# Optimization experiments

Hardware: AMD Instinct MI355X
Metric: run time of the kernel (lower is better)

The kernel has to match this reference:

```python
import jax, jax.numpy as jnp
import numpy as np

B, S, U = 4, 4096, 1024

def setup_inputs() -> dict:
    key = jax.random.key(0)
    ks = jax.random.split(key, 8)
    scale = 1.0 / np.sqrt(U)
    return {
        "query": jax.random.normal(ks[0], (B, S, U), dtype=jnp.float32),
        "key": jax.random.normal(ks[1], (B, S, U), dtype=jnp.float32),
        "value": jax.random.normal(ks[2], (B, S, U), dtype=jnp.float32),
        "mask": jnp.ones((B, S, 1), dtype=jnp.float32),
        "Wk": jax.random.normal(ks[3], (U, U), dtype=jnp.float32) * scale,
        "Wv": jax.random.normal(ks[4], (U, U), dtype=jnp.float32) * scale,
        "Wq": jax.random.normal(ks[5], (U, U), dtype=jnp.float32) * scale,
        "Wo": jax.random.normal(ks[6], (U, U), dtype=jnp.float32) * scale,
    }

def reference(query, key, value, mask, Wk, Wv, Wq, Wo):
    # Dense projections (no bias), per the keras layer
    pk = jnp.einsum('bsu,uv->bsv', key, Wk)
    pv = jnp.einsum('bsu,uv->bsv', value, Wv)
    pq = jnp.einsum('bsu,uv->bsv', query, Wq)
    # mask applied BEFORE swish on k, and to v
    pk = pk * mask
    pv = pv * mask
    pk = jax.nn.swish(pk)
    # kv = K^T V : [B, U, U]; out = Q @ kv : [B, S, U]
    kv = jnp.einsum('bsu,bsv->buv', pk, pv)
    out = jnp.einsum('bsu,buv->bsv', pq, kv)
    return jnp.einsum('bsu,uv->bsv', out, Wo)
```

## Files before the change

kernel.cpp:

```cpp
#include <hip/hip_runtime.h>
#include <cstdint>


typedef unsigned short u16;
typedef unsigned int   u32;
typedef float  f32x4  __attribute__((ext_vector_type(4)));
typedef __bf16 bf16x8 __attribute__((ext_vector_type(8)));
typedef u32    u32x4  __attribute__((ext_vector_type(4)));
typedef u16    u16x4  __attribute__((ext_vector_type(4)));

__device__ __forceinline__ u16 f2bf(float f) {
  u32 u = __builtin_bit_cast(u32, f);
  u = (u + 0x7FFFu + ((u >> 16) & 1u)) >> 16;
  return (u16)u;
}
__device__ __forceinline__ u32 pack2(float a, float b) {
  return (u32)f2bf(a) | ((u32)f2bf(b) << 16);
}

template<int EPI, int AF32>
__global__ __launch_bounds__(256)
void gemm_nt(const void* __restrict__ Aptr, const u16* __restrict__ Bptr,
             void* __restrict__ Cptr, const float* __restrict__ maskp,
             int M, int N, int K, int ldA, int ldB,
             long batchA, long batchB, long batchC)
{
  __shared__ u16 As[128 * 64];
  __shared__ u16 Bs[128 * 64];

  const int t    = threadIdx.x;
  const int z    = blockIdx.z;
  const int m0   = blockIdx.y * 128;
  const int n0   = blockIdx.x * 128;
  const int lane = t & 63;
  const int w    = t >> 6, wr = w >> 1, wc = w & 1;
  const int g    = lane >> 4, r16 = lane & 15;
  const int srow = t >> 3, sk8 = t & 7;
  const int swz_w = (sk8 ^ (srow & 7)) << 4;
  const int swz_r = (r16 & 7) << 4;

  const float* Af = (const float*)Aptr + (AF32 ? batchA * (long)z : 0);
  const u16*   Ab = (const u16*)Aptr   + (AF32 ? 0 : batchA * (long)z);
  const u16*   Bb = Bptr + batchB * (long)z;

  f32x4 acc[4][4];
  {
    f32x4 z4;
    for (int q = 0; q < 4; ++q) z4[q] = 0.f;
    #pragma unroll
    for (int i = 0; i < 4; ++i)
      #pragma unroll
      for (int j = 0; j < 4; ++j) acc[i][j] = z4;
  }

  f32x4 raf[4][2];
  u32x4 ra[4];
  u32x4 rb[4];

  auto LOAD = [&](int kt) {
    const long kcol = (long)kt * 64 + sk8 * 8;
    #pragma unroll
    for (int i = 0; i < 4; ++i) {
      const long arow = m0 + i * 32 + srow;
      if constexpr (AF32) {
        const float* p = Af + arow * (long)ldA + kcol;
        raf[i][0] = *(const f32x4*)p;
        raf[i][1] = *(const f32x4*)(p + 4);
      } else {
        const u16* p = Ab + arow * (long)ldA + kcol;
        ra[i] = *(const u32x4*)p;
      }
      const long brow = n0 + i * 32 + srow;
      rb[i] = *(const u32x4*)(Bb + brow * (long)ldB + kcol);
    }
  };

  auto STORE_LDS = [&]() {
    #pragma unroll
    for (int i = 0; i < 4; ++i) {
      const int off = (i * 32 + srow) * 128 + swz_w;
      if constexpr (AF32) {
        u32x4 v;
        v[0] = pack2(raf[i][0][0], raf[i][0][1]);
        v[1] = pack2(raf[i][0][2], raf[i][0][3]);
        v[2] = pack2(raf[i][1][0], raf[i][1][1]);
        v[3] = pack2(raf[i][1][2], raf[i][1][3]);
        *(u32x4*)((char*)As + off) = v;
      } else {
        *(u32x4*)((char*)As + off) = ra[i];
      }
      *(u32x4*)((char*)Bs + off) = rb[i];
    }
  };

  auto COMPUTE = [&]() {
    #pragma unroll
    for (int kk = 0; kk < 2; ++kk) {
      bf16x8 af[4], bfv[4];
      #pragma unroll
      for (int m = 0; m < 4; ++m) {
        const int row  = wr * 64 + m * 16 + r16;
        const int koff = (((kk * 4 + g) << 4) ^ swz_r);
        af[m] = *(const bf16x8*)((const char*)As + row * 128 + koff);
      }
      #pragma unroll
      for (int n = 0; n < 4; ++n) {
        const int row  = wc * 64 + n * 16 + r16;
        const int koff = (((kk * 4 + g) << 4) ^ swz_r);
        bfv[n] = *(const bf16x8*)((const char*)Bs + row * 128 + koff);
      }
      #pragma unroll
      for (int m = 0; m < 4; ++m)
        #pragma unroll
        for (int n = 0; n < 4; ++n)
          acc[m][n] = __builtin_amdgcn_mfma_f32_16x16x32_bf16(af[m], bfv[n], acc[m][n], 0, 0, 0);
    }
  };

  const int nk = K / 64;
  LOAD(0);
  for (int kt = 0;; ++kt) {
    __syncthreads();
    STORE_LDS();
    __syncthreads();
    if (kt + 1 < nk) LOAD(kt + 1);
    COMPUTE();
    if (kt + 1 >= nk) break;
  }

  if constexpr (EPI <= 1) {
    u16* C = (u16*)Cptr + batchC * (long)z;
    const float* mz = maskp + (long)z * M;
    #pragma unroll
    for (int m = 0; m < 4; ++m) {
      const int sbase = m0 + wr * 64 + m * 16 + 4 * g;
      float mk[4];
      #pragma unroll
      for (int j = 0; j < 4; ++j) mk[j] = mz[sbase + j];
      #pragma unroll
      for (int n = 0; n < 4; ++n) {
        const int col = n0 + wc * 64 + n * 16 + r16;
        u16x4 v;
        #pragma unroll
        for (int j = 0; j < 4; ++j) {
          float x = acc[m][n][j] * mk[j];
          if constexpr (EPI == 0) x = x / (1.f + __expf(-x));
          v[j] = f2bf(x);
        }
        *(u16x4*)(C + (long)col * M + sbase) = v;
      }
    }
  } else if constexpr (EPI == 2) {
    u16* C = (u16*)Cptr + batchC * (long)z;
    #pragma unroll
    for (int m = 0; m < 4; ++m) {
      const int rbase = m0 + wr * 64 + m * 16 + 4 * g;
      #pragma unroll
      for (int n = 0; n < 4; ++n) {
        const int col = n0 + wc * 64 + n * 16 + r16;
        #pragma unroll
        for (int j = 0; j < 4; ++j)
          C[(long)(rbase + j) * N + col] = f2bf(acc[m][n][j]);
      }
    }
  } else {
    float* C = (float*)Cptr + batchC * (long)z;
    #pragma unroll
    for (int m = 0; m < 4; ++m) {
      const int rbase = m0 + wr * 64 + m * 16 + 4 * g;
      #pragma unroll
      for (int n = 0; n < 4; ++n) {
        const int col = n0 + wc * 64 + n * 16 + r16;
        #pragma unroll
        for (int j = 0; j < 4; ++j)
          C[(long)(rbase + j) * N + col] = acc[m][n][j];
      }
    }
  }
}

__global__ void tconv_kernel(const float* __restrict__ src, u16* __restrict__ dst)
{
  __shared__ float tile[32][33];
  const int tx = threadIdx.x, ty = threadIdx.y;
  const int c0 = blockIdx.x * 32, r0 = blockIdx.y * 32;
  #pragma unroll
  for (int j = 0; j < 4; ++j)
    tile[ty * 4 + j][tx] = src[(long)(r0 + ty * 4 + j) * 1024 + c0 + tx];
  __syncthreads();
  #pragma unroll
  for (int j = 0; j < 4; ++j)
    dst[(long)(c0 + ty * 4 + j) * 1024 + r0 + tx] = f2bf(tile[tx][ty * 4 + j]);
}

__global__ void conv_kernel(const float* __restrict__ src, u16* __restrict__ dst, int n8)
{
  const int i = blockIdx.x * blockDim.x + threadIdx.x;
  if (i < n8) {
    const f32x4 a = *(const f32x4*)(src + (long)i * 8);
    const f32x4 b = *(const f32x4*)(src + (long)i * 8 + 4);
    u32x4 v;
    v[0] = pack2(a[0], a[1]);
    v[1] = pack2(a[2], a[3]);
    v[2] = pack2(b[0], b[1]);
    v[3] = pack2(b[2], b[3]);
    *(u32x4*)(dst + (long)i * 8) = v;
  }
}

extern "C" void kernel_launch(void* const* d_in, const int* in_sizes, int n_in,
                              void* d_out, int out_size, void* d_ws, size_t ws_size,
                              hipStream_t stream)
{
  const float* q    = (const float*)d_in[0];
  const float* k    = (const float*)d_in[1];
  const float* v    = (const float*)d_in[2];
  const float* mask = (const float*)d_in[3];
  const float* Wk   = (const float*)d_in[4];
  const float* Wv   = (const float*)d_in[5];
  const float* Wq   = (const float*)d_in[6];
  const float* Wo   = (const float*)d_in[7];

  const int B = 4, S = 4096, U = 1024;
  const long SU = (long)S * U;
  const long UU = (long)U * U;

  char* ws = (char*)d_ws;
  u16* pkT = (u16*)(ws);
  u16* pvT = (u16*)(ws + (32l << 20));
  u16* WkT = (u16*)(ws + (64l << 20));
  u16* WvT = (u16*)(ws + (66l << 20));
  u16* Wqb = (u16*)(ws + (68l << 20));
  u16* WoT = (u16*)(ws + (70l << 20));
  u16* kvT = (u16*)(ws + (72l << 20));
  u16* Wtm = (u16*)(ws + (80l << 20));
  u16* WfT = (u16*)(ws + (88l << 20));

  const dim3 blk(256);

  tconv_kernel<<<dim3(32, 32), dim3(32, 8), 0, stream>>>(Wk, WkT);
  tconv_kernel<<<dim3(32, 32), dim3(32, 8), 0, stream>>>(Wv, WvT);
  tconv_kernel<<<dim3(32, 32), dim3(32, 8), 0, stream>>>(Wo, WoT);
  conv_kernel<<<512, 256, 0, stream>>>(Wq, Wqb, (int)(UU / 8));

  gemm_nt<0, 1><<<dim3(8, 32, 4), blk, 0, stream>>>(k, WkT, pkT, mask,
      S, U, U, U, U, SU, 0, SU);
  gemm_nt<1, 1><<<dim3(8, 32, 4), blk, 0, stream>>>(v, WvT, pvT, mask,
      S, U, U, U, U, SU, 0, SU);
  gemm_nt<2, 0><<<dim3(8, 8, 4), blk, 0, stream>>>(pvT, pkT, kvT, nullptr,
      U, U, S, S, S, SU, SU, UU);
  gemm_nt<2, 0><<<dim3(8, 8, 4), blk, 0, stream>>>(Wqb, kvT, Wtm, nullptr,
      U, U, U, U, U, 0, UU, UU);
  gemm_nt<2, 0><<<dim3(8, 8, 4), blk, 0, stream>>>(WoT, Wtm, WfT, nullptr,
      U, U, U, U, U, 0, UU, UU);
  gemm_nt<3, 1><<<dim3(8, 32, 4), blk, 0, stream>>>(q, WfT, d_out, nullptr,
      S, U, U, U, U, SU, UU, SU);
}
```

Measured before the change: 504.5 us.

## Load GEMM tiles directly into LDS and pre-convert activations to bf16

The GEMM kernel now fills LDS with direct global-to-LDS 16-byte loads (global_load_lds) instead of staging through registers. It drops the XOR swizzle and the register prefetch of the next k-tile, so each iteration loads, waits, then computes. To allow this, the fp32 query/key/value inputs are first converted to bf16 by separate conversion passes, using the output buffer and freed workspace as scratch. The aim is to cut register staging and VGPR pressure. The costs are extra full-tensor conversion traffic, no load/compute overlap, and likely LDS bank conflicts on the unswizzled reads.

```diff
diff --git a/kernel.cpp b/kernel.cpp
--- a/kernel.cpp
+++ b/kernel.cpp
@@ -18,9 +18,16 @@
   return (u32)f2bf(a) | ((u32)f2bf(b) << 16);
 }
 
-template<int EPI, int AF32>
+__device__ __forceinline__ void gld_lds16(const u16* g, u16* l) {
+  __builtin_amdgcn_global_load_lds(
+      (const __attribute__((address_space(1))) void*)g,
+      (__attribute__((address_space(3))) void*)l,
+      16, 0, 0);
+}
+
+template<int EPI>
 __global__ __launch_bounds__(256)
-void gemm_nt(const void* __restrict__ Aptr, const u16* __restrict__ Bptr,
+void gemm_nt(const u16* __restrict__ Aptr, const u16* __restrict__ Bptr,
              void* __restrict__ Cptr, const float* __restrict__ maskp,
              int M, int N, int K, int ldA, int ldB,
              long batchA, long batchB, long batchC)
@@ -35,13 +42,15 @@
   const int lane = t & 63;
   const int w    = t >> 6, wr = w >> 1, wc = w & 1;
   const int g    = lane >> 4, r16 = lane & 15;
-  const int srow = t >> 3, sk8 = t & 7;
-  const int swz_w = (sk8 ^ (srow & 7)) << 4;
-  const int swz_r = (r16 & 7) << 4;
-
-  const float* Af = (const float*)Aptr + (AF32 ? batchA * (long)z : 0);
-  const u16*   Ab = (const u16*)Aptr   + (AF32 ? 0 : batchA * (long)z);
-  const u16*   Bb = Bptr + batchB * (long)z;
+  const int lrow = lane >> 3, lch = lane & 7;
+
+  const u16* Ab = Aptr + batchA * (long)z;
+  const u16* Bb = Bptr + batchB * (long)z;
+
+  const u16* pA = Ab + (long)(m0 + w * 32 + lrow) * ldA + lch * 8;
+  const u16* pB = Bb + (long)(n0 + w * 32 + lrow) * ldB + lch * 8;
+  u16* lA = As + w * 2048;
+  u16* lB = Bs + w * 2048;
 
   f32x4 acc[4][4];
   {
@@ -53,60 +62,30 @@
       for (int j = 0; j < 4; ++j) acc[i][j] = z4;
   }
 
-  f32x4 raf[4][2];
-  u32x4 ra[4];
-  u32x4 rb[4];
-
-  auto LOAD = [&](int kt) {
-    const long kcol = (long)kt * 64 + sk8 * 8;
-    #pragma unroll
-    for (int i = 0; i < 4; ++i) {
-      const long arow = m0 + i * 32 + srow;
-      if constexpr (AF32) {
-        const float* p = Af + arow * (long)ldA + kcol;
-        raf[i][0] = *(const f32x4*)p;
-        raf[i][1] = *(const f32x4*)(p + 4);
-      } else {
-        const u16* p = Ab + arow * (long)ldA + kcol;
-        ra[i] = *(const u32x4*)p;
-      }
-      const long brow = n0 + i * 32 + srow;
-      rb[i] = *(const u32x4*)(Bb + brow * (long)ldB + kcol);
-    }
-  };
-
-  auto STORE_LDS = [&]() {
-    #pragma unroll
-    for (int i = 0; i < 4; ++i) {
-      const int off = (i * 32 + srow) * 128 + swz_w;
-      if constexpr (AF32) {
-        u32x4 v;
-        v[0] = pack2(raf[i][0][0], raf[i][0][1]);
-        v[1] = pack2(raf[i][0][2], raf[i][0][3]);
-        v[2] = pack2(raf[i][1][0], raf[i][1][1]);
-        v[3] = pack2(raf[i][1][2], raf[i][1][3]);
-        *(u32x4*)((char*)As + off) = v;
-      } else {
-        *(u32x4*)((char*)As + off) = ra[i];
-      }
-      *(u32x4*)((char*)Bs + off) = rb[i];
-    }
-  };
-
-  auto COMPUTE = [&]() {
+  const int nk = K / 64;
+  for (int kt = 0; kt < nk; ++kt) {
+    __syncthreads();
+    const long ko = (long)kt * 64;
+    #pragma unroll
+    for (int j = 0; j < 4; ++j) {
+      gld_lds16(pA + (long)j * 8 * ldA + ko, lA + j * 512);
+      gld_lds16(pB + (long)j * 8 * ldB + ko, lB + j * 512);
+    }
+    asm volatile("s_waitcnt vmcnt(0)" ::: "memory");
+    __syncthreads();
     #pragma unroll
     for (int kk = 0; kk < 2; ++kk) {
       bf16x8 af[4], bfv[4];
       #pragma unroll
       for (int m = 0; m < 4; ++m) {
         const int row  = wr * 64 + m * 16 + r16;
-        const int koff = (((kk * 4 + g) << 4) ^ swz_r);
+        const int koff = (kk * 4 + g) << 4;
         af[m] = *(const bf16x8*)((const char*)As + row * 128 + koff);
       }
       #pragma unroll
       for (int n = 0; n < 4; ++n) {
         const int row  = wc * 64 + n * 16 + r16;
-        const int koff = (((kk * 4 + g) << 4) ^ swz_r);
+        const int koff = (kk * 4 + g) << 4;
         bfv[n] = *(const bf16x8*)((const char*)Bs + row * 128 + koff);
       }
       #pragma unroll
@@ -115,17 +94,6 @@
         for (int n = 0; n < 4; ++n)
           acc[m][n] = __builtin_amdgcn_mfma_f32_16x16x32_bf16(af[m], bfv[n], acc[m][n], 0, 0, 0);
     }
-  };
-
-  const int nk = K / 64;
-  LOAD(0);
-  for (int kt = 0;; ++kt) {
-    __syncthreads();
-    STORE_LDS();
-    __syncthreads();
-    if (kt + 1 < nk) LOAD(kt + 1);
-    COMPUTE();
-    if (kt + 1 >= nk) break;
   }
 
   if constexpr (EPI <= 1) {
@@ -221,38 +189,47 @@
   const float* Wq   = (const float*)d_in[6];
   const float* Wo   = (const float*)d_in[7];
 
-  const int B = 4, S = 4096, U = 1024;
+  const int S = 4096, U = 1024;
   const long SU = (long)S * U;
   const long UU = (long)U * U;
+  const long MB = 1l << 20;
+
+  u16* kb = (u16*)d_out;
+  u16* vb = (u16*)d_out + 4 * SU;
 
   char* ws = (char*)d_ws;
   u16* pkT = (u16*)(ws);
-  u16* pvT = (u16*)(ws + (32l << 20));
-  u16* WkT = (u16*)(ws + (64l << 20));
-  u16* WvT = (u16*)(ws + (66l << 20));
-  u16* Wqb = (u16*)(ws + (68l << 20));
-  u16* WoT = (u16*)(ws + (70l << 20));
-  u16* kvT = (u16*)(ws + (72l << 20));
-  u16* Wtm = (u16*)(ws + (80l << 20));
-  u16* WfT = (u16*)(ws + (88l << 20));
+  u16* qb  = (u16*)(ws);
+  u16* pvT = (u16*)(ws + 32 * MB);
+  u16* kvT = (u16*)(ws + 64 * MB);
+  u16* WfT = (u16*)(ws + 64 * MB);
+  u16* Wtm = (u16*)(ws + 72 * MB);
+  u16* WkT = (u16*)(ws + 80 * MB);
+  u16* WvT = (u16*)(ws + 82 * MB);
+  u16* Wqb = (u16*)(ws + 84 * MB);
+  u16* WoT = (u16*)(ws + 86 * MB);
 
   const dim3 blk(256);
+  const int n8_qkv = (int)(4 * SU / 8);
 
   tconv_kernel<<<dim3(32, 32), dim3(32, 8), 0, stream>>>(Wk, WkT);
   tconv_kernel<<<dim3(32, 32), dim3(32, 8), 0, stream>>>(Wv, WvT);
   tconv_kernel<<<dim3(32, 32), dim3(32, 8), 0, stream>>>(Wo, WoT);
   conv_kernel<<<512, 256, 0, stream>>>(Wq, Wqb, (int)(UU / 8));
 
-  gemm_nt<0, 1><<<dim3(8, 32, 4), blk, 0, stream>>>(k, WkT, pkT, mask,
+  conv_kernel<<<8192, 256, 0, stream>>>(k, kb, n8_qkv);
+  gemm_nt<0><<<dim3(8, 32, 4), blk, 0, stream>>>(kb, WkT, pkT, mask,
       S, U, U, U, U, SU, 0, SU);
-  gemm_nt<1, 1><<<dim3(8, 32, 4), blk, 0, stream>>>(v, WvT, pvT, mask,
+  conv_kernel<<<8192, 256, 0, stream>>>(v, vb, n8_qkv);
+  gemm_nt<1><<<dim3(8, 32, 4), blk, 0, stream>>>(vb, WvT, pvT, mask,
       S, U, U, U, U, SU, 0, SU);
-  gemm_nt<2, 0><<<dim3(8, 8, 4), blk, 0, stream>>>(pvT, pkT, kvT, nullptr,
+  gemm_nt<2><<<dim3(8, 8, 4), blk, 0, stream>>>(pvT, pkT, kvT, nullptr,
       U, U, S, S, S, SU, SU, UU);
-  gemm_nt<2, 0><<<dim3(8, 8, 4), blk, 0, stream>>>(Wqb, kvT, Wtm, nullptr,
+  conv_kernel<<<8192, 256, 0, stream>>>(q, qb, n8_qkv);
+  gemm_nt<2><<<dim3(8, 8, 4), blk, 0, stream>>>(Wqb, kvT, Wtm, nullptr,
       U, U, U, U, U, 0, UU, UU);
-  gemm_nt<2, 0><<<dim3(8, 8, 4), blk, 0, stream>>>(WoT, Wtm, WfT, nullptr,
+  gemm_nt<2><<<dim3(8, 8, 4), blk, 0, stream>>>(WoT, Wtm, WfT, nullptr,
       U, U, U, U, U, 0, UU, UU);
-  gemm_nt<3, 1><<<dim3(8, 32, 4), blk, 0, stream>>>(q, WfT, d_out, nullptr,
+  gemm_nt<3><<<dim3(8, 32, 4), blk, 0, stream>>>(qb, WfT, d_out, nullptr,
       S, U, U, U, U, SU, UU, SU);
 }
```

Result: slower. 545.2 us (+8.1%).
